# Kernel tuning notes

Measured on AMD Instinct MI355X. Metric: run time of the kernel, lower is better.

Reference implementation:

```python
import jax, jax.numpy as jnp
import numpy as np

B, SQ, SK = 2, 2048, 2048   # batch, n_query, n_memory
D, H, DFF = 1024, 16, 1024  # model dim, heads, ffn dim (must equal D per source constraints)
DH = D // H                 # head dim = 64
NEG = 1e9


def _split_heads(x):
    # (B, S, D) -> (B, H, S, DH)
    b, s, _ = x.shape
    return x.reshape(b, s, H, DH).transpose(0, 2, 1, 3)


def setup_inputs() -> dict:
    key = jax.random.key(0)
    ks = jax.random.split(key, 10)
    s = 0.02
    return {
        "q": jax.random.normal(ks[0], (B, SQ, D), jnp.float32),
        "k": jax.random.normal(ks[1], (B, SK, D), jnp.float32),
        "v": jax.random.normal(ks[2], (B, SK, D), jnp.float32),
        "Win_w": jax.random.normal(ks[3], (DFF, D), jnp.float32) * s,
        "Win_b": jnp.zeros((DFF,), jnp.float32),
        "Wff_w": jax.random.normal(ks[4], (D, DFF), jnp.float32) * s,
        "Wff_b": jnp.zeros((D,), jnp.float32),
        "Wout_w": jax.random.normal(ks[5], (D, D), jnp.float32) * s,
        "Wout_b": jnp.zeros((D,), jnp.float32),
        "attn_mask": jax.random.randint(ks[6], (B, SK), 0, 2, jnp.int32),
    }


def reference(q, k, v, Win_w, Win_b, Wff_w, Wff_b, Wout_w, Wout_b, attn_mask):
    # projections (in_linear; k,v additionally pass through out_linear as in source)
    qh = q @ Win_w.T + Win_b
    kh = (k @ Win_w.T + Win_b) @ Wout_w.T + Wout_b
    vh = (v @ Win_w.T + Win_b) @ Wout_w.T + Wout_b
    qh = qh * (D ** -0.5)

    qh, kh, vh = _split_heads(qh), _split_heads(kh), _split_heads(vh)

    # additive mask bias: 0 where mask==1, -1e9 where mask==0, broadcast over heads/queries
    bias = (attn_mask.astype(jnp.float32) - 1.0) * NEG  # (B, SK)
    scores = jnp.einsum("bhqd,bhkd->bhqk", qh, kh) + bias[:, None, None, :]
    probs = jax.nn.softmax(scores, axis=-1)
    out = jnp.einsum("bhqk,bhkd->bhqd", probs, vh)

    # merge heads: (B, H, SQ, DH) -> (B, SQ, D)
    out = out.transpose(0, 2, 1, 3).reshape(B, SQ, D)

    out = out @ Wff_w.T + Wff_b
    out = out @ Wout_w.T + Wout_b
    return out
```

## Files before the change

kernel.cpp:

```cpp
#include <hip/hip_runtime.h>
#include <cstdint>
#include <cstddef>

using u16 = unsigned short;
using u32 = unsigned int;

typedef __attribute__((ext_vector_type(8))) short short8;
typedef __attribute__((ext_vector_type(4))) float f32x4;

#define MFMA16(a, b, c) __builtin_amdgcn_mfma_f32_16x16x32_bf16((a), (b), (c), 0, 0, 0)

#define QSCALE 0.0450842200f

__device__ __forceinline__ u16 f2bf(float f) {
  u32 u = __float_as_uint(f);
  return (u16)((u + 0x7FFFu + ((u >> 16) & 1u)) >> 16);
}

__device__ __forceinline__ u32 pack_bf16(float a, float b) {
  u32 r;
  asm("v_cvt_pk_bf16_f32 %0, %1, %2" : "=v"(r) : "v"(a), "v"(b));
  return r;
}

__device__ __forceinline__ void gload_lds16(const u16* g, u16* l) {
  __builtin_amdgcn_global_load_lds((const __attribute__((address_space(1))) void*)g,
                                   (__attribute__((address_space(3))) void*)l, 16, 0, 0);
}

__global__ __launch_bounds__(256) void prep_all(
    const float* __restrict__ q, const float* __restrict__ k, const float* __restrict__ v,
    const float* __restrict__ Wout_w, const float* __restrict__ Win_w,
    const float* __restrict__ Wff_w, const float* __restrict__ Win_b,
    const float* __restrict__ Wout_b, u16* __restrict__ X,
    u16* __restrict__ Woutb, u16* __restrict__ Winb,
    u16* __restrict__ WinT, u16* __restrict__ WffT,
    float* __restrict__ bias2, float* __restrict__ bias1f) {
  __shared__ float tile[64][68];
  const int t = threadIdx.x;
  const int bid = blockIdx.x;
  if (bid < 12288) {
    int i4 = bid * 256 + t;
    const float* src = (i4 < 1048576) ? q : (i4 < 2097152) ? k : v;
    int loc = i4 & 1048575;
    float4 w = reinterpret_cast<const float4*>(src)[loc];
    u32 lo = (u32)f2bf(w.x) | ((u32)f2bf(w.y) << 16);
    u32 hi = (u32)f2bf(w.z) | ((u32)f2bf(w.w) << 16);
    reinterpret_cast<uint2*>(X)[i4] = make_uint2(lo, hi);
  } else if (bid < 14336) {
    const int wb = bid - 12288;
    const float* src = wb < 1024 ? Wout_w : Win_w;
    u16* dst = wb < 1024 ? Woutb : Winb;
    const float sc = wb < 1024 ? 1.0f : QSCALE;
    int i = (wb & 1023) * 256 + t;
    float4 vv = reinterpret_cast<const float4*>(src)[i];
    u32 lo = (u32)f2bf(vv.x * sc) | ((u32)f2bf(vv.y * sc) << 16);
    u32 hi = (u32)f2bf(vv.z * sc) | ((u32)f2bf(vv.w * sc) << 16);
    reinterpret_cast<uint2*>(dst)[i] = make_uint2(lo, hi);
  } else if (bid < 14848) {
    const int tb = bid - 14336;
    const float* in = tb < 256 ? Win_w : Wff_w;
    u16* out = tb < 256 ? WinT : WffT;
    const int tix = tb & 255;
    const int bx = (tix >> 4) * 64, by = (tix & 15) * 64;
    const int r = t >> 2, c16 = (t & 3) * 16;
#pragma unroll
    for (int i = 0; i < 4; ++i)
      *reinterpret_cast<float4*>(&tile[r][c16 + i * 4]) =
          *reinterpret_cast<const float4*>(&in[(size_t)(bx + r) * 1024 + by + c16 + i * 4]);
    __syncthreads();
    const int jj = t >> 2, i16 = (t & 3) * 16;
#pragma unroll
    for (int i = 0; i < 4; ++i) {
      uint2 p;
      p.x = (u32)f2bf(tile[i16 + i * 4 + 0][jj]) | ((u32)f2bf(tile[i16 + i * 4 + 1][jj]) << 16);
      p.y = (u32)f2bf(tile[i16 + i * 4 + 2][jj]) | ((u32)f2bf(tile[i16 + i * 4 + 3][jj]) << 16);
      *reinterpret_cast<uint2*>(&out[(size_t)(by + jj) * 1024 + bx + i16 + i * 4]) = p;
    }
  } else if (bid < 15104) {
    const int w = t >> 6, l = t & 63;
    const int j = (bid - 14848) * 4 + w;
    const float4* Wr = reinterpret_cast<const float4*>(Wout_w + (size_t)j * 1024);
    const float4* br = reinterpret_cast<const float4*>(Win_b);
    float s = 0.f;
    for (int i = l; i < 256; i += 64) {
      float4 a = Wr[i], b = br[i];
      s += a.x * b.x + a.y * b.y + a.z * b.z + a.w * b.w;
    }
#pragma unroll
    for (int o = 1; o < 64; o <<= 1) s += __shfl_xor(s, o);
    if (l == 0) bias2[j] = s + Wout_b[j];
  } else {
    float4 vv = reinterpret_cast<const float4*>(Win_b)[t];
    vv.x *= QSCALE; vv.y *= QSCALE; vv.z *= QSCALE; vv.w *= QSCALE;
    reinterpret_cast<float4*>(bias1f)[t] = vv;
  }
}

__global__ __launch_bounds__(256) void gemm_w2(const u16* __restrict__ A,
                                               const u16* __restrict__ Bt0,
                                               const u16* __restrict__ Bt1,
                                               u16* __restrict__ C0,
                                               u16* __restrict__ C1) {
  const int bid = blockIdx.x;
  const int xcd = bid & 7, local = bid >> 3;
  const int z = local >> 5;
  const int mt = xcd * 2 + ((local >> 4) & 1);
  const int nt = local & 15;
  const u16* Bt = z ? Bt1 : Bt0;
  u16* C = z ? C1 : C0;
  __shared__ __align__(16) u16 As[2][4096];
  __shared__ __align__(16) u16 Bs[2][4096];
  const int t = threadIdx.x, w = t >> 6, l = t & 63;
  const int l15 = l & 15, l4 = l >> 4;
  const int m0 = mt * 64, n0 = nt * 64;
  f32x4 acc[4] = {};
  const int row0 = t >> 3, cs0 = t & 7;
  const int c0 = cs0 ^ (row0 & 7);
  const int row1 = row0 + 32;
  const int c1 = cs0 ^ (row1 & 7);
  const u16* gA0 = A + (size_t)(m0 + row0) * 1024 + c0 * 8;
  const u16* gA1 = A + (size_t)(m0 + row1) * 1024 + c1 * 8;
  const u16* gB0 = Bt + (size_t)(n0 + row0) * 1024 + c0 * 8;
  const u16* gB1 = Bt + (size_t)(n0 + row1) * 1024 + c1 * 8;
#define W2_STAGE(KK, DST)                             \
  gload_lds16(gA0 + (KK), &As[DST][0] + w * 512);     \
  gload_lds16(gA1 + (KK), &As[DST][2048] + w * 512);  \
  gload_lds16(gB0 + (KK), &Bs[DST][0] + w * 512);     \
  gload_lds16(gB1 + (KK), &Bs[DST][2048] + w * 512);
  W2_STAGE(0, 0)
  for (int step = 0; step < 16; ++step) {
    const int c = step & 1;
    __syncthreads();
    if (step < 15) { W2_STAGE((step + 1) * 64, c ^ 1) }
#pragma unroll
    for (int ks = 0; ks < 2; ++ks) {
      const int cc = ks * 4 + l4;
      short8 bfr = *reinterpret_cast<const short8*>(&Bs[c][(w * 16 + l15) * 64 + ((cc ^ (l15 & 7)) * 8)]);
#pragma unroll
      for (int i = 0; i < 4; ++i) {
        short8 afr = *reinterpret_cast<const short8*>(&As[c][(i * 16 + l15) * 64 + ((cc ^ (l15 & 7)) * 8)]);
        acc[i] = MFMA16(afr, bfr, acc[i]);
      }
    }
  }
#pragma unroll
  for (int i = 0; i < 4; ++i)
#pragma unroll
    for (int j = 0; j < 4; ++j)
      C[(size_t)(m0 + i * 16 + l4 * 4 + j) * 1024 + n0 + w * 16 + l15] = f2bf(acc[i][j]);
}

__global__ __launch_bounds__(256) void proj(const u16* __restrict__ X,
                                            const u16* __restrict__ Winb,
                                            const u16* __restrict__ Wc2,
                                            const float* __restrict__ bias1f,
                                            const float* __restrict__ bias2,
                                            u16* __restrict__ Qh,
                                            u16* __restrict__ Kp,
                                            u16* __restrict__ VT) {
  __shared__ __align__(16) u16 As[2][4096];
  __shared__ __align__(16) u16 Bs[2][4096];
  const int t = threadIdx.x, w = t >> 6, l = t & 63;
  const int l15 = l & 15, l4 = l >> 4;
  const int bid = blockIdx.x;
  const int xcd = bid & 7, local = bid >> 3;
  const int mt = xcd * 12 + (local >> 3);
  const int nt = local & 7;
  const int seg = mt >> 5;
  const int m0 = mt * 128;
  const int n0 = nt * 128;
  const int wr = (w >> 1) * 64, wc = (w & 1) * 64;
  const u16* Bt = seg == 0 ? Winb : Wc2;
  const float* bias = seg == 0 ? bias1f : bias2;

  f32x4 acc[4][4] = {};
  const int srow = t >> 2;
  const int sck = (t & 3) ^ ((t >> 3) & 3);
  const u16* gA = X + (size_t)(m0 + srow) * 1024 + sck * 8;
  const u16* gB = Bt + (size_t)(n0 + srow) * 1024 + sck * 8;
#define PJ_STAGE(KK, DST)                                   \
  gload_lds16(gA + (KK), &As[DST][0] + w * 512);            \
  gload_lds16(gA + (KK) + 65536, &As[DST][2048] + w * 512); \
  gload_lds16(gB + (KK), &Bs[DST][0] + w * 512);            \
  gload_lds16(gB + (KK) + 65536, &Bs[DST][2048] + w * 512);
  PJ_STAGE(0, 0)
  const int sw = (l15 >> 1) & 3;
  for (int step = 0; step < 32; ++step) {
    const int c = step & 1;
    __syncthreads();
    if (step < 31) { PJ_STAGE((step + 1) * 32, c ^ 1) }
    short8 af[4], bf[4];
#pragma unroll
    for (int i = 0; i < 4; ++i)
      af[i] = *reinterpret_cast<const short8*>(&As[c][(wr + i * 16 + l15) * 32 + ((l4 ^ sw) * 8)]);
#pragma unroll
    for (int i = 0; i < 4; ++i)
      bf[i] = *reinterpret_cast<const short8*>(&Bs[c][(wc + i * 16 + l15) * 32 + ((l4 ^ sw) * 8)]);
#pragma unroll
    for (int mi = 0; mi < 4; ++mi)
#pragma unroll
      for (int ni = 0; ni < 4; ++ni)
        acc[mi][ni] = MFMA16(af[mi], bf[ni], acc[mi][ni]);
  }

#pragma unroll
  for (int mi = 0; mi < 4; ++mi) {
#pragma unroll
    for (int ni = 0; ni < 4; ++ni) {
      const int col = n0 + wc + ni * 16 + l15;
      const float bv = bias[col];
      const int row0 = m0 + wr + mi * 16 + l4 * 4;
      if (seg == 0) {
#pragma unroll
        for (int j = 0; j < 4; ++j)
          Qh[(size_t)(row0 + j) * 1024 + col] = f2bf(acc[mi][ni][j] + bv);
      } else if (seg == 1) {
#pragma unroll
        for (int j = 0; j < 4; ++j)
          Kp[(size_t)(row0 - 4096 + j) * 1024 + col] = f2bf(acc[mi][ni][j] + bv);
      } else {
        const int r = row0 - 8192;
        const int bb = r >> 11;
        const int sk = r & 2047;
        u32 p0 = (u32)f2bf(acc[mi][ni][0] + bv) | ((u32)f2bf(acc[mi][ni][1] + bv) << 16);
        u32 p1 = (u32)f2bf(acc[mi][ni][2] + bv) | ((u32)f2bf(acc[mi][ni][3] + bv) << 16);
        *reinterpret_cast<uint2*>(VT + ((size_t)(bb * 1024 + col)) * 2048 + sk) = make_uint2(p0, p1);
      }
    }
  }
}

__global__ __launch_bounds__(512) void attn(const u16* __restrict__ Qh,
                                            const u16* __restrict__ Kb,
                                            const u16* __restrict__ VT,
                                            const int* __restrict__ mask,
                                            u16* __restrict__ AO,
                                            const float* __restrict__ Wout_w,
                                            const float* __restrict__ Wff_b,
                                            const float* __restrict__ Wout_b,
                                            float* __restrict__ bias3) {
  __shared__ __align__(16) u16 Kt[128 * 64];
  __shared__ __align__(16) u16 Vt[2][64 * 64];
  __shared__ float biasS[2048];
  const int t = threadIdx.x, l = t & 63, w = t >> 6;
  const int bid = blockIdx.x;

  if (bid >= 512) {
    const int j = (bid - 512) * 8 + w;
    const float4* Wr = reinterpret_cast<const float4*>(Wout_w + (size_t)j * 1024);
    const float4* br = reinterpret_cast<const float4*>(Wff_b);
    float s = 0.f;
    for (int i = l; i < 256; i += 64) {
      float4 a = Wr[i], b = br[i];
      s += a.x * b.x + a.y * b.y + a.z * b.z + a.w * b.w;
    }
#pragma unroll
    for (int o = 1; o < 64; o <<= 1) s += __shfl_xor(s, o);
    if (l == 0) bias3[j] = s + Wout_b[j];
    return;
  }

  const int l15 = l & 15, l4 = l >> 4;
  const int bh = (bid & 7) * 4 + ((bid >> 3) & 3);
  const int qb = bid >> 5;
  const int b = bh >> 4, h = bh & 15, q0 = qb * 128;

  for (int i = t; i < 2048; i += 512) biasS[i] = mask[b * 2048 + i] ? 0.f : -1.442695e9f;

  short8 qf[2];
  {
    const u16* qp = Qh + (size_t)(b * 2048 + q0 + w * 16 + l15) * 1024 + h * 64 + l4 * 8;
    qf[0] = *reinterpret_cast<const short8*>(qp);
    qf[1] = *reinterpret_cast<const short8*>(qp + 32);
  }
  short8 ones;
#pragma unroll
  for (int i = 0; i < 8; ++i) ones[i] = (short)0x3F80;

  f32x4 acc[4] = {};
  f32x4 accS = {};

  const int rr = t >> 3, cs = t & 7;
  const int ck = cs ^ (rr & 7);
  const int vb = (ck >> 2) * 32 + (ck & 3) * 4;
  const u16* gK = Kb + (size_t)(b * 2048 + rr) * 1024 + h * 64 + ck * 8;
  u16* ldsK = Kt + w * 512;
  const u32* gVrow = reinterpret_cast<const u32*>(VT) + (size_t)(b * 1024 + h * 64 + rr) * 1024;

  for (int kt = 0; kt < 2048; kt += 128) {
    const int ia = (kt >> 1) + (vb >> 1);
    uint2 a01 = *reinterpret_cast<const uint2*>(gVrow + ia);
    uint2 a89 = *reinterpret_cast<const uint2*>(gVrow + ia + 8);
    uint2 b01 = *reinterpret_cast<const uint2*>(gVrow + ia + 32);
    uint2 b89 = *reinterpret_cast<const uint2*>(gVrow + ia + 40);
    __syncthreads();
    gload_lds16(gK + (size_t)kt * 1024, ldsK);
    gload_lds16(gK + (size_t)(kt + 64) * 1024, ldsK + 4096);
    *reinterpret_cast<uint4*>(&Vt[0][rr * 64 + cs * 8]) = make_uint4(a01.x, a01.y, a89.x, a89.y);
    *reinterpret_cast<uint4*>(&Vt[1][rr * 64 + cs * 8]) = make_uint4(b01.x, b01.y, b89.x, b89.y);
    __syncthreads();

#pragma unroll
    for (int half = 0; half < 2; ++half) {
      const int kb0 = kt + half * 64;
      f32x4 s[4];
#pragma unroll
      for (int n = 0; n < 4; ++n)
        s[n] = *reinterpret_cast<const f32x4*>(&biasS[kb0 + n * 16 + l4 * 4]);
      __builtin_amdgcn_s_setprio(1);
#pragma unroll
      for (int ks = 0; ks < 2; ++ks) {
        const int cc = ks * 4 + l4;
#pragma unroll
        for (int n = 0; n < 4; ++n) {
          short8 kb = *reinterpret_cast<const short8*>(
              &Kt[(half * 64 + n * 16 + l15) * 64 + ((cc ^ (l15 & 7)) * 8)]);
          s[n] = MFMA16(kb, qf[ks], s[n]);
        }
      }
      __builtin_amdgcn_s_setprio(0);
#pragma unroll
      for (int n = 0; n < 4; ++n)
#pragma unroll
        for (int j = 0; j < 4; ++j) s[n][j] = __builtin_amdgcn_exp2f(s[n][j]);
      u32 paw[8];
      paw[0] = pack_bf16(s[0][0], s[0][1]);
      paw[1] = pack_bf16(s[0][2], s[0][3]);
      paw[2] = pack_bf16(s[1][0], s[1][1]);
      paw[3] = pack_bf16(s[1][2], s[1][3]);
      paw[4] = pack_bf16(s[2][0], s[2][1]);
      paw[5] = pack_bf16(s[2][2], s[2][3]);
      paw[6] = pack_bf16(s[3][0], s[3][1]);
      paw[7] = pack_bf16(s[3][2], s[3][3]);
      const short8 pa0 = *reinterpret_cast<const short8*>(&paw[0]);
      const short8 pa1 = *reinterpret_cast<const short8*>(&paw[4]);
      __builtin_amdgcn_s_setprio(1);
#pragma unroll
      for (int ks = 0; ks < 2; ++ks) {
        const short8 pa = ks ? pa1 : pa0;
        const int cc = ks * 4 + l4;
#pragma unroll
        for (int n = 0; n < 4; ++n) {
          short8 vb8 = *reinterpret_cast<const short8*>(
              &Vt[half][(n * 16 + l15) * 64 + ((cc ^ (l15 & 7)) * 8)]);
          acc[n] = MFMA16(pa, vb8, acc[n]);
        }
        accS = MFMA16(pa, ones, accS);
      }
      __builtin_amdgcn_s_setprio(0);
    }
  }

  const size_t orow0 = (size_t)(b * 2048 + q0 + w * 16 + l4 * 4);
#pragma unroll
  for (int j = 0; j < 4; ++j) {
    const float inv = 1.0f / accS[j];
#pragma unroll
    for (int n = 0; n < 4; ++n)
      AO[(orow0 + j) * 1024 + h * 64 + n * 16 + l15] = f2bf(acc[n][j] * inv);
  }
}

__global__ __launch_bounds__(256) void gemm_tail(const u16* __restrict__ A,
                                                 const u16* __restrict__ Bt,
                                                 const float* __restrict__ bias,
                                                 float* __restrict__ C) {
  __shared__ __align__(16) u16 As[2][4096];
  __shared__ __align__(16) u16 Bs[2][2048];
  const int t = threadIdx.x, w = t >> 6, l = t & 63;
  const int l15 = l & 15, l4 = l >> 4;
  const int bid = blockIdx.x;
  const int xcd = bid & 7, local = bid >> 3;
  const int mt = xcd * 4 + (local >> 4);
  const int nt = local & 15;
  const int m0 = mt * 128, n0 = nt * 64;
  const int wr = (w >> 1) * 64, wc = (w & 1) * 32;
  f32x4 acc[4][2] = {};
  const int srow = t >> 2;
  const int sck = (t & 3) ^ ((t >> 3) & 3);
  const u16* gA = A + (size_t)(m0 + srow) * 1024 + sck * 8;
  const u16* gB = Bt + (size_t)(n0 + srow) * 1024 + sck * 8;
#define TL_STAGE(KK, DST)                                   \
  gload_lds16(gA + (KK), &As[DST][0] + w * 512);            \
  gload_lds16(gA + (KK) + 65536, &As[DST][2048] + w * 512); \
  gload_lds16(gB + (KK), &Bs[DST][0] + w * 512);
  TL_STAGE(0, 0)
  const int sw = (l15 >> 1) & 3;
  for (int step = 0; step < 32; ++step) {
    const int c = step & 1;
    __syncthreads();
    if (step < 31) { TL_STAGE((step + 1) * 32, c ^ 1) }
    short8 af[4], bf[2];
#pragma unroll
    for (int i = 0; i < 4; ++i)
      af[i] = *reinterpret_cast<const short8*>(&As[c][(wr + i * 16 + l15) * 32 + ((l4 ^ sw) * 8)]);
#pragma unroll
    for (int i = 0; i < 2; ++i)
      bf[i] = *reinterpret_cast<const short8*>(&Bs[c][(wc + i * 16 + l15) * 32 + ((l4 ^ sw) * 8)]);
#pragma unroll
    for (int mi = 0; mi < 4; ++mi)
#pragma unroll
      for (int ni = 0; ni < 2; ++ni)
        acc[mi][ni] = MFMA16(af[mi], bf[ni], acc[mi][ni]);
  }
#pragma unroll
  for (int mi = 0; mi < 4; ++mi) {
#pragma unroll
    for (int ni = 0; ni < 2; ++ni) {
      const int col = n0 + wc + ni * 16 + l15;
      const float bv = bias[col];
      const int row0 = m0 + wr + mi * 16 + l4 * 4;
#pragma unroll
      for (int j = 0; j < 4; ++j)
        C[(size_t)(row0 + j) * 1024 + col] = acc[mi][ni][j] + bv;
    }
  }
}

extern "C" void kernel_launch(void* const* d_in, const int* in_sizes, int n_in,
                              void* d_out, int out_size, void* d_ws, size_t ws_size,
                              hipStream_t stream) {
  const float* q = (const float*)d_in[0];
  const float* k = (const float*)d_in[1];
  const float* v = (const float*)d_in[2];
  const float* Win_w = (const float*)d_in[3];
  const float* Win_b = (const float*)d_in[4];
  const float* Wff_w = (const float*)d_in[5];
  const float* Wff_b = (const float*)d_in[6];
  const float* Wout_w = (const float*)d_in[7];
  const float* Wout_b = (const float*)d_in[8];
  const int* mask = (const int*)d_in[9];
  float* out = (float*)d_out;

  char* ws = (char*)d_ws;
  u16* Xbf = (u16*)ws;
  u16* AO = (u16*)ws;
  float* bias3 = (float*)(ws + 20971520);
  u16* Qh = (u16*)(ws + 25165824);
  u16* WinT = (u16*)(ws + 25165824);
  u16* Woutb = (u16*)(ws + 27262976);
  u16* WffT = (u16*)(ws + 29360128);
  u16* Kproj = (u16*)(ws + 33554432);
  u16* VT = (u16*)(ws + 41943040);
  u16* Wc2 = (u16*)(ws + 50331648);
  u16* Wc3 = (u16*)(ws + 52428800);
  u16* Winb = (u16*)(ws + 54525952);
  float* bias2 = out;
  float* bias1f = out + 1024;

  prep_all<<<15105, 256, 0, stream>>>(q, k, v, Wout_w, Win_w, Wff_w, Win_b, Wout_b,
                                      Xbf, Woutb, Winb, WinT, WffT, bias2, bias1f);
  gemm_w2<<<512, 256, 0, stream>>>(Woutb, WinT, WffT, Wc2, Wc3);
  proj<<<768, 256, 0, stream>>>(Xbf, Winb, Wc2, bias1f, bias2, Qh, Kproj, VT);
  attn<<<640, 512, 0, stream>>>(Qh, Kproj, VT, mask, AO, Wout_w, Wff_b, Wout_b, bias3);
  gemm_tail<<<512, 256, 0, stream>>>(AO, Wc3, bias3, out);
}
```

Measured before the change: 140.9 us.

## Halve attention block size and give each wave two 16-row query groups

The attention kernel now runs 256-thread blocks where each wave handles 32 query rows (two 16-row groups) instead of 16. Each K and V fragment read from LDS is reused for twice as many MFMAs, and each thread loads twice as much of the K/V tile. The intent is to cut LDS read traffic per MFMA and raise instruction-level parallelism. The cost is more registers per thread (doubled accumulators and scores), which may lower occupancy. The bias-precompute blocks are resized to match (768 blocks, 4 rows each).

```diff
diff --git a/kernel.cpp b/kernel.cpp
--- a/kernel.cpp
+++ b/kernel.cpp
@@ -231,7 +231,7 @@
   }
 }
 
-__global__ __launch_bounds__(512) void attn(const u16* __restrict__ Qh,
+__global__ __launch_bounds__(256) void attn(const u16* __restrict__ Qh,
                                             const u16* __restrict__ Kb,
                                             const u16* __restrict__ VT,
                                             const int* __restrict__ mask,
@@ -247,7 +247,7 @@
   const int bid = blockIdx.x;
 
   if (bid >= 512) {
-    const int j = (bid - 512) * 8 + w;
+    const int j = (bid - 512) * 4 + w;
     const float4* Wr = reinterpret_cast<const float4*>(Wout_w + (size_t)j * 1024);
     const float4* br = reinterpret_cast<const float4*>(Wff_b);
     float s = 0.f;
@@ -266,48 +266,64 @@
   const int qb = bid >> 5;
   const int b = bh >> 4, h = bh & 15, q0 = qb * 128;
 
-  for (int i = t; i < 2048; i += 512) biasS[i] = mask[b * 2048 + i] ? 0.f : -1.442695e9f;
-
-  short8 qf[2];
-  {
-    const u16* qp = Qh + (size_t)(b * 2048 + q0 + w * 16 + l15) * 1024 + h * 64 + l4 * 8;
-    qf[0] = *reinterpret_cast<const short8*>(qp);
-    qf[1] = *reinterpret_cast<const short8*>(qp + 32);
+  for (int i = t; i < 2048; i += 256) biasS[i] = mask[b * 2048 + i] ? 0.f : -1.442695e9f;
+
+  short8 qf[2][2];
+#pragma unroll
+  for (int qg = 0; qg < 2; ++qg) {
+    const u16* qp =
+        Qh + (size_t)(b * 2048 + q0 + w * 32 + qg * 16 + l15) * 1024 + h * 64 + l4 * 8;
+    qf[qg][0] = *reinterpret_cast<const short8*>(qp);
+    qf[qg][1] = *reinterpret_cast<const short8*>(qp + 32);
   }
   short8 ones;
 #pragma unroll
   for (int i = 0; i < 8; ++i) ones[i] = (short)0x3F80;
 
-  f32x4 acc[4] = {};
-  f32x4 accS = {};
+  f32x4 acc[2][4] = {};
+  f32x4 accS[2] = {};
 
   const int rr = t >> 3, cs = t & 7;
   const int ck = cs ^ (rr & 7);
   const int vb = (ck >> 2) * 32 + (ck & 3) * 4;
   const u16* gK = Kb + (size_t)(b * 2048 + rr) * 1024 + h * 64 + ck * 8;
   u16* ldsK = Kt + w * 512;
-  const u32* gVrow = reinterpret_cast<const u32*>(VT) + (size_t)(b * 1024 + h * 64 + rr) * 1024;
+  const u32* gV0 = reinterpret_cast<const u32*>(VT) + (size_t)(b * 1024 + h * 64 + rr) * 1024;
+  const u32* gV1 = gV0 + (size_t)32 * 1024;
 
   for (int kt = 0; kt < 2048; kt += 128) {
     const int ia = (kt >> 1) + (vb >> 1);
-    uint2 a01 = *reinterpret_cast<const uint2*>(gVrow + ia);
-    uint2 a89 = *reinterpret_cast<const uint2*>(gVrow + ia + 8);
-    uint2 b01 = *reinterpret_cast<const uint2*>(gVrow + ia + 32);
-    uint2 b89 = *reinterpret_cast<const uint2*>(gVrow + ia + 40);
+    uint2 a01 = *reinterpret_cast<const uint2*>(gV0 + ia);
+    uint2 a89 = *reinterpret_cast<const uint2*>(gV0 + ia + 8);
+    uint2 b01 = *reinterpret_cast<const uint2*>(gV0 + ia + 32);
+    uint2 b89 = *reinterpret_cast<const uint2*>(gV0 + ia + 40);
+    uint2 c01 = *reinterpret_cast<const uint2*>(gV1 + ia);
+    uint2 c89 = *reinterpret_cast<const uint2*>(gV1 + ia + 8);
+    uint2 d01 = *reinterpret_cast<const uint2*>(gV1 + ia + 32);
+    uint2 d89 = *reinterpret_cast<const uint2*>(gV1 + ia + 40);
     __syncthreads();
     gload_lds16(gK + (size_t)kt * 1024, ldsK);
+    gload_lds16(gK + (size_t)(kt + 32) * 1024, ldsK + 2048);
     gload_lds16(gK + (size_t)(kt + 64) * 1024, ldsK + 4096);
+    gload_lds16(gK + (size_t)(kt + 96) * 1024, ldsK + 6144);
     *reinterpret_cast<uint4*>(&Vt[0][rr * 64 + cs * 8]) = make_uint4(a01.x, a01.y, a89.x, a89.y);
+    *reinterpret_cast<uint4*>(&Vt[0][(rr + 32) * 64 + cs * 8]) =
+        make_uint4(c01.x, c01.y, c89.x, c89.y);
     *reinterpret_cast<uint4*>(&Vt[1][rr * 64 + cs * 8]) = make_uint4(b01.x, b01.y, b89.x, b89.y);
+    *reinterpret_cast<uint4*>(&Vt[1][(rr + 32) * 64 + cs * 8]) =
+        make_uint4(d01.x, d01.y, d89.x, d89.y);
     __syncthreads();
 
 #pragma unroll
     for (int half = 0; half < 2; ++half) {
       const int kb0 = kt + half * 64;
-      f32x4 s[4];
-#pragma unroll
-      for (int n = 0; n < 4; ++n)
-        s[n] = *reinterpret_cast<const f32x4*>(&biasS[kb0 + n * 16 + l4 * 4]);
+      f32x4 s[4][2];
+#pragma unroll
+      for (int n = 0; n < 4; ++n) {
+        f32x4 bv4 = *reinterpret_cast<const f32x4*>(&biasS[kb0 + n * 16 + l4 * 4]);
+        s[n][0] = bv4;
+        s[n][1] = bv4;
+      }
       __builtin_amdgcn_s_setprio(1);
 #pragma unroll
       for (int ks = 0; ks < 2; ++ks) {
@@ -316,49 +332,60 @@
         for (int n = 0; n < 4; ++n) {
           short8 kb = *reinterpret_cast<const short8*>(
               &Kt[(half * 64 + n * 16 + l15) * 64 + ((cc ^ (l15 & 7)) * 8)]);
-          s[n] = MFMA16(kb, qf[ks], s[n]);
+          s[n][0] = MFMA16(kb, qf[0][ks], s[n][0]);
+          s[n][1] = MFMA16(kb, qf[1][ks], s[n][1]);
         }
       }
       __builtin_amdgcn_s_setprio(0);
 #pragma unroll
       for (int n = 0; n < 4; ++n)
 #pragma unroll
-        for (int j = 0; j < 4; ++j) s[n][j] = __builtin_amdgcn_exp2f(s[n][j]);
-      u32 paw[8];
-      paw[0] = pack_bf16(s[0][0], s[0][1]);
-      paw[1] = pack_bf16(s[0][2], s[0][3]);
-      paw[2] = pack_bf16(s[1][0], s[1][1]);
-      paw[3] = pack_bf16(s[1][2], s[1][3]);
-      paw[4] = pack_bf16(s[2][0], s[2][1]);
-      paw[5] = pack_bf16(s[2][2], s[2][3]);
-      paw[6] = pack_bf16(s[3][0], s[3][1]);
-      paw[7] = pack_bf16(s[3][2], s[3][3]);
-      const short8 pa0 = *reinterpret_cast<const short8*>(&paw[0]);
-      const short8 pa1 = *reinterpret_cast<const short8*>(&paw[4]);
+        for (int qg = 0; qg < 2; ++qg)
+#pragma unroll
+          for (int j = 0; j < 4; ++j) s[n][qg][j] = __builtin_amdgcn_exp2f(s[n][qg][j]);
+      short8 pa[2][2];
+#pragma unroll
+      for (int qg = 0; qg < 2; ++qg) {
+        u32 paw[8];
+        paw[0] = pack_bf16(s[0][qg][0], s[0][qg][1]);
+        paw[1] = pack_bf16(s[0][qg][2], s[0][qg][3]);
+        paw[2] = pack_bf16(s[1][qg][0], s[1][qg][1]);
+        paw[3] = pack_bf16(s[1][qg][2], s[1][qg][3]);
+        paw[4] = pack_bf16(s[2][qg][0], s[2][qg][1]);
+        paw[5] = pack_bf16(s[2][qg][2], s[2][qg][3]);
+        paw[6] = pack_bf16(s[3][qg][0], s[3][qg][1]);
+        paw[7] = pack_bf16(s[3][qg][2], s[3][qg][3]);
+        pa[qg][0] = *reinterpret_cast<const short8*>(&paw[0]);
+        pa[qg][1] = *reinterpret_cast<const short8*>(&paw[4]);
+      }
       __builtin_amdgcn_s_setprio(1);
 #pragma unroll
       for (int ks = 0; ks < 2; ++ks) {
-        const short8 pa = ks ? pa1 : pa0;
         const int cc = ks * 4 + l4;
 #pragma unroll
         for (int n = 0; n < 4; ++n) {
           short8 vb8 = *reinterpret_cast<const short8*>(
               &Vt[half][(n * 16 + l15) * 64 + ((cc ^ (l15 & 7)) * 8)]);
-          acc[n] = MFMA16(pa, vb8, acc[n]);
+          acc[0][n] = MFMA16(pa[0][ks], vb8, acc[0][n]);
+          acc[1][n] = MFMA16(pa[1][ks], vb8, acc[1][n]);
         }
-        accS = MFMA16(pa, ones, accS);
+        accS[0] = MFMA16(pa[0][ks], ones, accS[0]);
+        accS[1] = MFMA16(pa[1][ks], ones, accS[1]);
       }
       __builtin_amdgcn_s_setprio(0);
     }
   }
 
-  const size_t orow0 = (size_t)(b * 2048 + q0 + w * 16 + l4 * 4);
-#pragma unroll
-  for (int j = 0; j < 4; ++j) {
-    const float inv = 1.0f / accS[j];
-#pragma unroll
-    for (int n = 0; n < 4; ++n)
-      AO[(orow0 + j) * 1024 + h * 64 + n * 16 + l15] = f2bf(acc[n][j] * inv);
+#pragma unroll
+  for (int qg = 0; qg < 2; ++qg) {
+    const size_t orow0 = (size_t)(b * 2048 + q0 + w * 32 + qg * 16 + l4 * 4);
+#pragma unroll
+    for (int j = 0; j < 4; ++j) {
+      const float inv = 1.0f / accS[qg][j];
+#pragma unroll
+      for (int n = 0; n < 4; ++n)
+        AO[(orow0 + j) * 1024 + h * 64 + n * 16 + l15] = f2bf(acc[qg][n][j] * inv);
+    }
   }
 }
 
@@ -453,6 +480,6 @@
                                       Xbf, Woutb, Winb, WinT, WffT, bias2, bias1f);
   gemm_w2<<<512, 256, 0, stream>>>(Woutb, WinT, WffT, Wc2, Wc3);
   proj<<<768, 256, 0, stream>>>(Xbf, Winb, Wc2, bias1f, bias2, Qh, Kproj, VT);
-  attn<<<640, 512, 0, stream>>>(Qh, Kproj, VT, mask, AO, Wout_w, Wff_b, Wout_b, bias3);
+  attn<<<768, 256, 0, stream>>>(Qh, Kproj, VT, mask, AO, Wout_w, Wff_b, Wout_b, bias3);
   gemm_tail<<<512, 256, 0, stream>>>(AO, Wc3, bias3, out);
 }
```

Result: slower. 144.9 us (+2.8%).

## Move activation bf16 conversion into weight-GEMM kernel to overlap with it

Applied to the files above, without the earlier changes.

The fp32-to-bf16 conversion of q/k/v now lives in the weight-product GEMM kernel instead of the weight prep kernel. Extra blocks beyond the first 512 do the conversion, so the memory-bound conversion can run alongside the small weight GEMM rather than before it. The prep kernel shrinks to weight-only work. The trade-off is that the GEMM kernel now declares LDS for every block, which may reduce how many conversion blocks fit on each CU.

```diff
diff --git a/kernel.cpp b/kernel.cpp
--- a/kernel.cpp
+++ b/kernel.cpp
@@ -28,37 +28,27 @@
                                    (__attribute__((address_space(3))) void*)l, 16, 0, 0);
 }
 
-__global__ __launch_bounds__(256) void prep_all(
-    const float* __restrict__ q, const float* __restrict__ k, const float* __restrict__ v,
+__global__ __launch_bounds__(256) void prep_w(
     const float* __restrict__ Wout_w, const float* __restrict__ Win_w,
     const float* __restrict__ Wff_w, const float* __restrict__ Win_b,
-    const float* __restrict__ Wout_b, u16* __restrict__ X,
+    const float* __restrict__ Wout_b,
     u16* __restrict__ Woutb, u16* __restrict__ Winb,
     u16* __restrict__ WinT, u16* __restrict__ WffT,
     float* __restrict__ bias2, float* __restrict__ bias1f) {
   __shared__ float tile[64][68];
   const int t = threadIdx.x;
   const int bid = blockIdx.x;
-  if (bid < 12288) {
-    int i4 = bid * 256 + t;
-    const float* src = (i4 < 1048576) ? q : (i4 < 2097152) ? k : v;
-    int loc = i4 & 1048575;
-    float4 w = reinterpret_cast<const float4*>(src)[loc];
-    u32 lo = (u32)f2bf(w.x) | ((u32)f2bf(w.y) << 16);
-    u32 hi = (u32)f2bf(w.z) | ((u32)f2bf(w.w) << 16);
-    reinterpret_cast<uint2*>(X)[i4] = make_uint2(lo, hi);
-  } else if (bid < 14336) {
-    const int wb = bid - 12288;
-    const float* src = wb < 1024 ? Wout_w : Win_w;
-    u16* dst = wb < 1024 ? Woutb : Winb;
-    const float sc = wb < 1024 ? 1.0f : QSCALE;
-    int i = (wb & 1023) * 256 + t;
+  if (bid < 2048) {
+    const float* src = bid < 1024 ? Wout_w : Win_w;
+    u16* dst = bid < 1024 ? Woutb : Winb;
+    const float sc = bid < 1024 ? 1.0f : QSCALE;
+    int i = (bid & 1023) * 256 + t;
     float4 vv = reinterpret_cast<const float4*>(src)[i];
     u32 lo = (u32)f2bf(vv.x * sc) | ((u32)f2bf(vv.y * sc) << 16);
     u32 hi = (u32)f2bf(vv.z * sc) | ((u32)f2bf(vv.w * sc) << 16);
     reinterpret_cast<uint2*>(dst)[i] = make_uint2(lo, hi);
-  } else if (bid < 14848) {
-    const int tb = bid - 14336;
+  } else if (bid < 2560) {
+    const int tb = bid - 2048;
     const float* in = tb < 256 ? Win_w : Wff_w;
     u16* out = tb < 256 ? WinT : WffT;
     const int tix = tb & 255;
@@ -77,9 +67,9 @@
       p.y = (u32)f2bf(tile[i16 + i * 4 + 2][jj]) | ((u32)f2bf(tile[i16 + i * 4 + 3][jj]) << 16);
       *reinterpret_cast<uint2*>(&out[(size_t)(by + jj) * 1024 + bx + i16 + i * 4]) = p;
     }
-  } else if (bid < 15104) {
+  } else if (bid < 2816) {
     const int w = t >> 6, l = t & 63;
-    const int j = (bid - 14848) * 4 + w;
+    const int j = (bid - 2560) * 4 + w;
     const float4* Wr = reinterpret_cast<const float4*>(Wout_w + (size_t)j * 1024);
     const float4* br = reinterpret_cast<const float4*>(Win_b);
     float s = 0.f;
@@ -97,21 +87,36 @@
   }
 }
 
-__global__ __launch_bounds__(256) void gemm_w2(const u16* __restrict__ A,
-                                               const u16* __restrict__ Bt0,
-                                               const u16* __restrict__ Bt1,
-                                               u16* __restrict__ C0,
-                                               u16* __restrict__ C1) {
+__global__ __launch_bounds__(256) void w2_cvt(const u16* __restrict__ A,
+                                              const u16* __restrict__ Bt0,
+                                              const u16* __restrict__ Bt1,
+                                              u16* __restrict__ C0,
+                                              u16* __restrict__ C1,
+                                              const float* __restrict__ q,
+                                              const float* __restrict__ k,
+                                              const float* __restrict__ v,
+                                              u16* __restrict__ X) {
+  __shared__ __align__(16) u16 As[2][4096];
+  __shared__ __align__(16) u16 Bs[2][4096];
   const int bid = blockIdx.x;
+  const int t = threadIdx.x;
+  if (bid >= 512) {
+    int i4 = (bid - 512) * 256 + t;
+    const float* src = (i4 < 1048576) ? q : (i4 < 2097152) ? k : v;
+    int loc = i4 & 1048575;
+    float4 w4 = reinterpret_cast<const float4*>(src)[loc];
+    u32 lo = (u32)f2bf(w4.x) | ((u32)f2bf(w4.y) << 16);
+    u32 hi = (u32)f2bf(w4.z) | ((u32)f2bf(w4.w) << 16);
+    reinterpret_cast<uint2*>(X)[i4] = make_uint2(lo, hi);
+    return;
+  }
   const int xcd = bid & 7, local = bid >> 3;
   const int z = local >> 5;
   const int mt = xcd * 2 + ((local >> 4) & 1);
   const int nt = local & 15;
   const u16* Bt = z ? Bt1 : Bt0;
   u16* C = z ? C1 : C0;
-  __shared__ __align__(16) u16 As[2][4096];
-  __shared__ __align__(16) u16 Bs[2][4096];
-  const int t = threadIdx.x, w = t >> 6, l = t & 63;
+  const int w = t >> 6, l = t & 63;
   const int l15 = l & 15, l4 = l >> 4;
   const int m0 = mt * 64, n0 = nt * 64;
   f32x4 acc[4] = {};
@@ -449,9 +454,9 @@
   float* bias2 = out;
   float* bias1f = out + 1024;
 
-  prep_all<<<15105, 256, 0, stream>>>(q, k, v, Wout_w, Win_w, Wff_w, Win_b, Wout_b,
-                                      Xbf, Woutb, Winb, WinT, WffT, bias2, bias1f);
-  gemm_w2<<<512, 256, 0, stream>>>(Woutb, WinT, WffT, Wc2, Wc3);
+  prep_w<<<2817, 256, 0, stream>>>(Wout_w, Win_w, Wff_w, Win_b, Wout_b,
+                                   Woutb, Winb, WinT, WffT, bias2, bias1f);
+  w2_cvt<<<12800, 256, 0, stream>>>(Woutb, WinT, WffT, Wc2, Wc3, q, k, v, Xbf);
   proj<<<768, 256, 0, stream>>>(Xbf, Winb, Wc2, bias1f, bias2, Qh, Kproj, VT);
   attn<<<640, 512, 0, stream>>>(Qh, Kproj, VT, mask, AO, Wout_w, Wff_b, Wout_b, bias3);
   gemm_tail<<<512, 256, 0, stream>>>(AO, Wc3, bias3, out);
```

Result: faster. 137.8 us (median of 2 runs) (-2.2%).
